# Performance work log

Hardware: AMD Instinct MI355X
Metric: run time of the kernel (lower is better)

Reference implementation:

```python
import jax, jax.numpy as jnp
import numpy as np

ROUTING_ITERS = 3

def _squash(s, axis=-1):
    # v = s * ||s||^2 / (1 + ||s||^2) / ||s||
    n2 = jnp.sum(s * s, axis=axis, keepdims=True)
    return s * n2 / (1.0 + n2) / jnp.sqrt(n2 + 1e-8)

def setup_inputs() -> dict:
    key = jax.random.key(0)
    k1, k2, k3 = jax.random.split(key, 3)
    B, R, C, O, I = 256, 1152, 10, 16, 8
    x = jax.random.normal(k1, (B, R, I), dtype=jnp.float32)
    W = jax.random.normal(k2, (R, C, O, I), dtype=jnp.float32) * 0.05
    bias = jax.random.normal(k3, (C, O), dtype=jnp.float32) * 0.05
    return {"x": x, "W": W, "bias": bias}

def reference(x, W, bias):
    # x: [B,R,I], W: [R,C,O,I], bias: [C,O]
    B = x.shape[0]
    R, C, O, I = W.shape
    # u_hat[b,r,c,o] = W[r,c,o,:] . x[b,r,:]   (torch: matmul(W, x) over broadcast batch)
    u_hat = jnp.einsum('rcoi,bri->brco', W, x)  # [B,R,C,O]
    b_ij = jnp.zeros((R, C), dtype=x.dtype)
    v = None
    for it in range(ROUTING_ITERS):
        c_ij = jax.nn.softmax(b_ij, axis=1)  # softmax over capsules (dim=2 in torch layout)
        s = jnp.einsum('rc,brco->bco', c_ij, u_hat) + bias  # [B,C,O]
        v = _squash(s, axis=-1)  # squash over out_channels (dim=-2 of [B,1,C,O,1])
        if it < ROUTING_ITERS - 1:
            # agreement: u_hat^T v, then mean over batch (keepdim collapses to shared logits)
            agree = jnp.einsum('brco,bco->brc', u_hat, v).mean(axis=0)  # [R,C]
            b_ij = b_ij + agree
    # torch returns v_j.squeeze(1): [B, C, O, 1]
    return v[..., None]
```

## Files before the change

### kernel.cpp

```cpp
#include <hip/hip_runtime.h>

#define CB 256
#define CR 1152
#define CC 10
#define CO 16
#define CI 8
#define CK (CR*CI)
#define NCO (CC*CO)

typedef __bf16 bf16_t;
typedef __attribute__((ext_vector_type(8))) __bf16 bf16x8;
typedef __attribute__((ext_vector_type(4))) float f32x4;

__global__ __launch_bounds__(256) void k_cvt(const float* __restrict__ x,
                                             const float* __restrict__ W,
                                             bf16_t* __restrict__ xb,
                                             bf16_t* __restrict__ xTb,
                                             bf16_t* __restrict__ Wt) {
  const int t = threadIdx.x;
  if (blockIdx.x < 1152) {
    const int bt = blockIdx.x & 7, kt = blockIdx.x >> 3;
    const int b0 = bt * 32, k0 = kt * 64;
    __shared__ float ldsT[64][33];
    const int row = t >> 3, cv = t & 7;
    const float4* xp = (const float4*)(x + (size_t)(b0 + row) * CK + k0 + cv * 8);
    const float4 f0 = xp[0], f1 = xp[1];
    float vals[8] = {f0.x, f0.y, f0.z, f0.w, f1.x, f1.y, f1.z, f1.w};
    bf16x8 ov;
    #pragma unroll
    for (int j = 0; j < 8; ++j) {
      ov[j] = (bf16_t)vals[j];
      ldsT[cv * 8 + j][row] = vals[j];
    }
    *(bf16x8*)(xb + (size_t)(b0 + row) * CK + k0 + cv * 8) = ov;
    __syncthreads();
    const int kr = t >> 2, bs = t & 3;
    bf16x8 tv;
    #pragma unroll
    for (int j = 0; j < 8; ++j) tv[j] = (bf16_t)ldsT[kr][bs * 8 + j];
    *(bf16x8*)(xTb + (size_t)(k0 + kr) * CB + b0 + bs * 8) = tv;
  } else {
    const int wi = (blockIdx.x - 1152) * 256 + t;
    const int r = wi % CR;
    const int co = wi / CR;
    const int c = co >> 4, o = co & 15;
    const float4* src = (const float4*)(W + (((size_t)r * CC + c) * CO + o) * CI);
    const float4 f0 = src[0], f1 = src[1];
    bf16x8 v;
    v[0] = (bf16_t)f0.x; v[1] = (bf16_t)f0.y; v[2] = (bf16_t)f0.z; v[3] = (bf16_t)f0.w;
    v[4] = (bf16_t)f1.x; v[5] = (bf16_t)f1.y; v[6] = (bf16_t)f1.z; v[7] = (bf16_t)f1.w;
    *(bf16x8*)(Wt + (size_t)co * CK + r * 8) = v;
  }
}

template<int MODE, bool LAST>
__global__ __launch_bounds__(1024) void k_s(const bf16_t* __restrict__ xb,
                                            const bf16_t* __restrict__ Bmat,
                                            const float* __restrict__ bias,
                                            bf16_t* __restrict__ vTb,
                                            float* __restrict__ out) {
  const int blk = blockIdx.x;
  const int xcd = blk & 7, j = blk >> 3;
  const int bt = xcd * 2 + (j & 1);
  const int c = j >> 1;
  const int t = threadIdx.x;
  const int w = t >> 6, lane = t & 63;
  const int mrow = lane & 15, kg = lane >> 4;
  const int b0 = bt * 16;
  const size_t kbase = (size_t)w * (CK / 16);

  const bf16x8* ap = (const bf16x8*)(xb + (size_t)(b0 + mrow) * CK + kbase) + kg;
  const bf16x8* bp = (const bf16x8*)(Bmat + (size_t)(c * CO + mrow) * CK + kbase) + kg;

  f32x4 acc0 = {0.f, 0.f, 0.f, 0.f}, acc1 = {0.f, 0.f, 0.f, 0.f};
  #pragma unroll
  for (int s = 0; s < 18; s += 2) {
    acc0 = __builtin_amdgcn_mfma_f32_16x16x32_bf16(ap[s * 4], bp[s * 4], acc0, 0, 0, 0);
    acc1 = __builtin_amdgcn_mfma_f32_16x16x32_bf16(ap[(s + 1) * 4], bp[(s + 1) * 4], acc1, 0, 0, 0);
  }
  const f32x4 acc = acc0 + acc1;

  __shared__ float Ls[16][64][4];
  #pragma unroll
  for (int reg = 0; reg < 4; ++reg) Ls[w][lane][reg] = acc[reg];
  __syncthreads();

  if (t < 256) {
    const int row = t >> 4, col = t & 15;
    const int l = ((row >> 2) << 4) | col, reg = row & 3;
    float s = 0.f;
    #pragma unroll
    for (int q = 0; q < 16; ++q) s += Ls[q][l][reg];
    if (MODE == 0) s *= 0.1f;
    s += bias[c * CO + col];
    float n2 = s * s;
    #pragma unroll
    for (int m = 1; m < 16; m <<= 1) n2 += __shfl_xor(n2, m);
    const float vv = s * n2 / (1.f + n2) * rsqrtf(n2 + 1e-8f);
    if (LAST) out[(size_t)(b0 + row) * NCO + c * CO + col] = vv;
    else      vTb[(size_t)(c * CO + col) * CB + b0 + row] = (bf16_t)vv;
  }
}

template<bool FIRST>
__global__ __launch_bounds__(512) void k_asc(const bf16_t* __restrict__ xTb,
                                             const bf16_t* __restrict__ vTb,
                                             const float* __restrict__ W,
                                             const bf16_t* __restrict__ Wt,
                                             float* __restrict__ b_ij,
                                             bf16_t* __restrict__ Wts) {
  const int r0 = blockIdx.x * 8;
  const int t = threadIdx.x;
  const int h = t >> 8;
  const int th = t & 255;
  const int w = th >> 6, lane = th & 63;
  const int mrow = lane & 15, kg = lane >> 4;

  __shared__ __align__(16) unsigned short vL[NCO][CB + 8];
  __shared__ float agrL[8][CC];
  __shared__ float cwL[8][CC];

  #pragma unroll
  for (int q = 0; q < 10; ++q) {
    const int idx = q * 512 + t;
    const int co = idx >> 5, bs = idx & 31;
    const bf16x8 v = ((const bf16x8*)vTb)[idx];
    *(bf16x8*)&vL[co][bs * 8] = v;
  }

  const int m0 = r0 * 8 + w * 16;
  const bf16x8* ap = (const bf16x8*)(xTb + (size_t)(m0 + mrow) * CB) + kg;
  bf16x8 a[8];
  #pragma unroll
  for (int s = 0; s < 8; ++s) a[s] = ap[s * 4];
  __syncthreads();

  const int o = lane & 15, g = lane >> 4;
  #pragma unroll
  for (int cc = 0; cc < 5; ++cc) {
    const int c = h * 5 + cc;
    f32x4 acc = {0.f, 0.f, 0.f, 0.f};
    #pragma unroll
    for (int s = 0; s < 8; ++s) {
      const bf16x8 bv = *(const bf16x8*)&vL[c * CO + mrow][s * 32 + kg * 8];
      acc = __builtin_amdgcn_mfma_f32_16x16x32_bf16(a[s], bv, acc, 0, 0, 0);
    }
    float p = 0.f;
    #pragma unroll
    for (int reg = 0; reg < 4; ++reg) {
      const int m = g * 4 + reg, rl = m >> 3, i = m & 7;
      p += acc[reg] * W[(((size_t)(r0 + w * 2 + rl) * CC + c) * CO + o) * CI + i];
    }
    #pragma unroll
    for (int msk = 1; msk < 32; msk <<= 1) p += __shfl_xor(p, msk);
    if ((lane & 31) == 0) agrL[w * 2 + (lane >> 5)][c] = p * (1.0f / CB);
  }
  __syncthreads();

  if (t < 8) {
    const int r = r0 + t;
    float nb[CC];
    float mx = -1e30f;
    #pragma unroll
    for (int c = 0; c < CC; ++c) {
      nb[c] = (FIRST ? 0.f : b_ij[r * CC + c]) + agrL[t][c];
      mx = fmaxf(mx, nb[c]);
    }
    float sum = 0.f;
    #pragma unroll
    for (int c = 0; c < CC; ++c) {
      b_ij[r * CC + c] = nb[c];
      const float e = __expf(nb[c] - mx);
      cwL[t][c] = e;
      sum += e;
    }
    const float inv = 1.f / sum;
    #pragma unroll
    for (int c = 0; c < CC; ++c) cwL[t][c] *= inv;
  }
  __syncthreads();

  #pragma unroll
  for (int q = 0; q < 3; ++q) {
    const int slot = q * 512 + t;
    if (slot < 1280) {
      const int co = slot >> 3, rl = slot & 7;
      const float cw = cwL[rl][co >> 4];
      const size_t off = (size_t)co * CK + (r0 + rl) * 8;
      const bf16x8 wv = *(const bf16x8*)(Wt + off);
      bf16x8 ov;
      #pragma unroll
      for (int jj = 0; jj < 8; ++jj) ov[jj] = (bf16_t)((float)wv[jj] * cw);
      *(bf16x8*)(Wts + off) = ov;
    }
  }
}

extern "C" void kernel_launch(void* const* d_in, const int* in_sizes, int n_in,
                              void* d_out, int out_size, void* d_ws, size_t ws_size,
                              hipStream_t stream) {
  const float* x    = (const float*)d_in[0];
  const float* W    = (const float*)d_in[1];
  const float* bias = (const float*)d_in[2];
  float* out = (float*)d_out;

  bf16_t* xb  = (bf16_t*)d_ws;
  bf16_t* xTb = xb  + (size_t)CB * CK;
  bf16_t* Wt  = xTb + (size_t)CB * CK;
  bf16_t* Wts = Wt  + (size_t)NCO * CK;
  bf16_t* vTb = Wts + (size_t)NCO * CK;
  float*  b_ij = (float*)(vTb + (size_t)NCO * CB);

  k_cvt<<<1872, 256, 0, stream>>>(x, W, xb, xTb, Wt);

  k_s<0, false><<<160, 1024, 0, stream>>>(xb, Wt, bias, vTb, out);
  k_asc<true><<<144, 512, 0, stream>>>(xTb, vTb, W, Wt, b_ij, Wts);

  k_s<1, false><<<160, 1024, 0, stream>>>(xb, Wts, bias, vTb, out);
  k_asc<false><<<144, 512, 0, stream>>>(xTb, vTb, W, Wt, b_ij, Wts);

  k_s<1, true><<<160, 1024, 0, stream>>>(xb, Wts, bias, vTb, out);
}
```

Baseline: 86.13 us.

## Fuse bf16 conversion into routing kernels and drop precomputed weight copies

New measurement: 103.9 us. +20.6%, slower.

```diff
diff --git a/kernel.cpp b/kernel.cpp
--- a/kernel.cpp
+++ b/kernel.cpp
@@ -12,75 +12,59 @@
 typedef __attribute__((ext_vector_type(8))) __bf16 bf16x8;
 typedef __attribute__((ext_vector_type(4))) float f32x4;
 
-__global__ __launch_bounds__(256) void k_cvt(const float* __restrict__ x,
-                                             const float* __restrict__ W,
-                                             bf16_t* __restrict__ xb,
-                                             bf16_t* __restrict__ xTb,
-                                             bf16_t* __restrict__ Wt) {
-  const int t = threadIdx.x;
-  if (blockIdx.x < 1152) {
-    const int bt = blockIdx.x & 7, kt = blockIdx.x >> 3;
-    const int b0 = bt * 32, k0 = kt * 64;
-    __shared__ float ldsT[64][33];
-    const int row = t >> 3, cv = t & 7;
-    const float4* xp = (const float4*)(x + (size_t)(b0 + row) * CK + k0 + cv * 8);
-    const float4 f0 = xp[0], f1 = xp[1];
-    float vals[8] = {f0.x, f0.y, f0.z, f0.w, f1.x, f1.y, f1.z, f1.w};
-    bf16x8 ov;
-    #pragma unroll
-    for (int j = 0; j < 8; ++j) {
-      ov[j] = (bf16_t)vals[j];
-      ldsT[cv * 8 + j][row] = vals[j];
-    }
-    *(bf16x8*)(xb + (size_t)(b0 + row) * CK + k0 + cv * 8) = ov;
-    __syncthreads();
-    const int kr = t >> 2, bs = t & 3;
-    bf16x8 tv;
-    #pragma unroll
-    for (int j = 0; j < 8; ++j) tv[j] = (bf16_t)ldsT[kr][bs * 8 + j];
-    *(bf16x8*)(xTb + (size_t)(k0 + kr) * CB + b0 + bs * 8) = tv;
-  } else {
-    const int wi = (blockIdx.x - 1152) * 256 + t;
-    const int r = wi % CR;
-    const int co = wi / CR;
-    const int c = co >> 4, o = co & 15;
-    const float4* src = (const float4*)(W + (((size_t)r * CC + c) * CO + o) * CI);
-    const float4 f0 = src[0], f1 = src[1];
-    bf16x8 v;
-    v[0] = (bf16_t)f0.x; v[1] = (bf16_t)f0.y; v[2] = (bf16_t)f0.z; v[3] = (bf16_t)f0.w;
-    v[4] = (bf16_t)f1.x; v[5] = (bf16_t)f1.y; v[6] = (bf16_t)f1.z; v[7] = (bf16_t)f1.w;
-    *(bf16x8*)(Wt + (size_t)co * CK + r * 8) = v;
-  }
+__device__ __forceinline__ unsigned short bfbits(float f) {
+  union { __bf16 h; unsigned short u; } u; u.h = (bf16_t)f; return u.u;
 }
 
 template<int MODE, bool LAST>
-__global__ __launch_bounds__(1024) void k_s(const bf16_t* __restrict__ xb,
-                                            const bf16_t* __restrict__ Bmat,
-                                            const float* __restrict__ bias,
-                                            bf16_t* __restrict__ vTb,
-                                            float* __restrict__ out) {
+__global__ __launch_bounds__(512) void k_s(const float* __restrict__ x,
+                                           const float* __restrict__ W,
+                                           const float* __restrict__ bias,
+                                           const float* __restrict__ cwT,
+                                           bf16_t* __restrict__ vTb,
+                                           float* __restrict__ out) {
   const int blk = blockIdx.x;
   const int xcd = blk & 7, j = blk >> 3;
-  const int bt = xcd * 2 + (j & 1);
-  const int c = j >> 1;
+  const int bt = (xcd & 3) * 4 + (j & 3);
+  const int c  = (xcd >> 2) * 5 + (j >> 2);
   const int t = threadIdx.x;
   const int w = t >> 6, lane = t & 63;
   const int mrow = lane & 15, kg = lane >> 4;
   const int b0 = bt * 16;
-  const size_t kbase = (size_t)w * (CK / 16);
 
-  const bf16x8* ap = (const bf16x8*)(xb + (size_t)(b0 + mrow) * CK + kbase) + kg;
-  const bf16x8* bp = (const bf16x8*)(Bmat + (size_t)(c * CO + mrow) * CK + kbase) + kg;
+  __shared__ float cwS[CR];
+  __shared__ float Ls[8][64][4];
+  if (MODE == 1) {
+    if (t < CR / 4) ((float4*)cwS)[t] = ((const float4*)(cwT + (size_t)c * CR))[t];
+    __syncthreads();
+  }
 
-  f32x4 acc0 = {0.f, 0.f, 0.f, 0.f}, acc1 = {0.f, 0.f, 0.f, 0.f};
-  #pragma unroll
-  for (int s = 0; s < 18; s += 2) {
-    acc0 = __builtin_amdgcn_mfma_f32_16x16x32_bf16(ap[s * 4], bp[s * 4], acc0, 0, 0, 0);
-    acc1 = __builtin_amdgcn_mfma_f32_16x16x32_bf16(ap[(s + 1) * 4], bp[(s + 1) * 4], acc1, 0, 0, 0);
+  const int r0w = w * 144;
+  const float4* ax = (const float4*)(x + (size_t)(b0 + mrow) * CK + (size_t)w * 1152) + kg * 2;
+
+  f32x4 acc = {0.f, 0.f, 0.f, 0.f};
+  #pragma unroll 4
+  for (int s = 0; s < 36; ++s) {
+    const float4 a0 = ax[s * 8], a1 = ax[s * 8 + 1];
+    const int r = r0w + s * 4 + kg;
+    const float4* wp = (const float4*)(W + (((size_t)r * CC + c) * CO + mrow) * CI);
+    const float4 w0 = wp[0], w1 = wp[1];
+    bf16x8 af, bf;
+    af[0] = (bf16_t)a0.x; af[1] = (bf16_t)a0.y; af[2] = (bf16_t)a0.z; af[3] = (bf16_t)a0.w;
+    af[4] = (bf16_t)a1.x; af[5] = (bf16_t)a1.y; af[6] = (bf16_t)a1.z; af[7] = (bf16_t)a1.w;
+    if (MODE == 1) {
+      const float cw = cwS[r];
+      bf[0] = (bf16_t)(w0.x * cw); bf[1] = (bf16_t)(w0.y * cw);
+      bf[2] = (bf16_t)(w0.z * cw); bf[3] = (bf16_t)(w0.w * cw);
+      bf[4] = (bf16_t)(w1.x * cw); bf[5] = (bf16_t)(w1.y * cw);
+      bf[6] = (bf16_t)(w1.z * cw); bf[7] = (bf16_t)(w1.w * cw);
+    } else {
+      bf[0] = (bf16_t)w0.x; bf[1] = (bf16_t)w0.y; bf[2] = (bf16_t)w0.z; bf[3] = (bf16_t)w0.w;
+      bf[4] = (bf16_t)w1.x; bf[5] = (bf16_t)w1.y; bf[6] = (bf16_t)w1.z; bf[7] = (bf16_t)w1.w;
+    }
+    acc = __builtin_amdgcn_mfma_f32_16x16x32_bf16(af, bf, acc, 0, 0, 0);
   }
-  const f32x4 acc = acc0 + acc1;
 
-  __shared__ float Ls[16][64][4];
   #pragma unroll
   for (int reg = 0; reg < 4; ++reg) Ls[w][lane][reg] = acc[reg];
   __syncthreads();
@@ -90,7 +74,7 @@
     const int l = ((row >> 2) << 4) | col, reg = row & 3;
     float s = 0.f;
     #pragma unroll
-    for (int q = 0; q < 16; ++q) s += Ls[q][l][reg];
+    for (int q = 0; q < 8; ++q) s += Ls[q][l][reg];
     if (MODE == 0) s *= 0.1f;
     s += bias[c * CO + col];
     float n2 = s * s;
@@ -103,12 +87,11 @@
 }
 
 template<bool FIRST>
-__global__ __launch_bounds__(512) void k_asc(const bf16_t* __restrict__ xTb,
+__global__ __launch_bounds__(512) void k_asc(const float* __restrict__ x,
+                                             const float* __restrict__ W,
                                              const bf16_t* __restrict__ vTb,
-                                             const float* __restrict__ W,
-                                             const bf16_t* __restrict__ Wt,
                                              float* __restrict__ b_ij,
-                                             bf16_t* __restrict__ Wts) {
+                                             float* __restrict__ cwT) {
   const int r0 = blockIdx.x * 8;
   const int t = threadIdx.x;
   const int h = t >> 8;
@@ -117,6 +100,7 @@
   const int mrow = lane & 15, kg = lane >> 4;
 
   __shared__ __align__(16) unsigned short vL[NCO][CB + 8];
+  __shared__ __align__(16) unsigned short xTl[64][CB + 8];
   __shared__ float agrL[8][CC];
   __shared__ float cwL[8][CC];
 
@@ -127,13 +111,20 @@
     const bf16x8 v = ((const bf16x8*)vTb)[idx];
     *(bf16x8*)&vL[co][bs * 8] = v;
   }
+  #pragma unroll
+  for (int chunk = 0; chunk < 16; ++chunk) {
+    const int b = chunk * 16 + (t >> 5);
+    const int ri = (t & 31) * 2;
+    const float2 v = *(const float2*)(x + (size_t)b * CK + r0 * 8 + ri);
+    xTl[ri][b] = bfbits(v.x);
+    xTl[ri + 1][b] = bfbits(v.y);
+  }
+  __syncthreads();
 
-  const int m0 = r0 * 8 + w * 16;
-  const bf16x8* ap = (const bf16x8*)(xTb + (size_t)(m0 + mrow) * CB) + kg;
   bf16x8 a[8];
   #pragma unroll
-  for (int s = 0; s < 8; ++s) a[s] = ap[s * 4];
-  __syncthreads();
+  for (int s = 0; s < 8; ++s)
+    a[s] = *(const bf16x8*)&xTl[w * 16 + mrow][s * 32 + kg * 8];
 
   const int o = lane & 15, g = lane >> 4;
   #pragma unroll
@@ -176,23 +167,7 @@
     }
     const float inv = 1.f / sum;
     #pragma unroll
-    for (int c = 0; c < CC; ++c) cwL[t][c] *= inv;
-  }
-  __syncthreads();
-
-  #pragma unroll
-  for (int q = 0; q < 3; ++q) {
-    const int slot = q * 512 + t;
-    if (slot < 1280) {
-      const int co = slot >> 3, rl = slot & 7;
-      const float cw = cwL[rl][co >> 4];
-      const size_t off = (size_t)co * CK + (r0 + rl) * 8;
-      const bf16x8 wv = *(const bf16x8*)(Wt + off);
-      bf16x8 ov;
-      #pragma unroll
-      for (int jj = 0; jj < 8; ++jj) ov[jj] = (bf16_t)((float)wv[jj] * cw);
-      *(bf16x8*)(Wts + off) = ov;
-    }
+    for (int c = 0; c < CC; ++c) cwT[(size_t)c * CR + r] = cwL[t][c] * inv;
   }
 }
 
@@ -204,20 +179,15 @@
   const float* bias = (const float*)d_in[2];
   float* out = (float*)d_out;
 
-  bf16_t* xb  = (bf16_t*)d_ws;
-  bf16_t* xTb = xb  + (size_t)CB * CK;
-  bf16_t* Wt  = xTb + (size_t)CB * CK;
-  bf16_t* Wts = Wt  + (size_t)NCO * CK;
-  bf16_t* vTb = Wts + (size_t)NCO * CK;
+  bf16_t* vTb  = (bf16_t*)d_ws;
   float*  b_ij = (float*)(vTb + (size_t)NCO * CB);
+  float*  cwT  = b_ij + (size_t)CR * CC;
 
-  k_cvt<<<1872, 256, 0, stream>>>(x, W, xb, xTb, Wt);
+  k_s<0, false><<<160, 512, 0, stream>>>(x, W, bias, cwT, vTb, out);
+  k_asc<true><<<144, 512, 0, stream>>>(x, W, vTb, b_ij, cwT);
 
-  k_s<0, false><<<160, 1024, 0, stream>>>(xb, Wt, bias, vTb, out);
-  k_asc<true><<<144, 512, 0, stream>>>(xTb, vTb, W, Wt, b_ij, Wts);
+  k_s<1, false><<<160, 512, 0, stream>>>(x, W, bias, cwT, vTb, out);
+  k_asc<false><<<144, 512, 0, stream>>>(x, W, vTb, b_ij, cwT);
 
-  k_s<1, false><<<160, 1024, 0, stream>>>(xb, Wts, bias, vTb, out);
-  k_asc<false><<<144, 512, 0, stream>>>(xTb, vTb, W, Wt, b_ij, Wts);
-
-  k_s<1, true><<<160, 1024, 0, stream>>>(xb, Wts, bias, vTb, out);
+  k_s<1, true><<<160, 512, 0, stream>>>(x, W, bias, cwT, vTb, out);
 }
```

## Drop global transposed x copy; transpose x into LDS inside agreement kernel

Applied to the files above, without the earlier changes.

Measured after the change: 85.14 us. No clear change (-1.1%).

```diff
diff --git a/kernel.cpp b/kernel.cpp
--- a/kernel.cpp
+++ b/kernel.cpp
@@ -12,39 +12,28 @@
 typedef __attribute__((ext_vector_type(8))) __bf16 bf16x8;
 typedef __attribute__((ext_vector_type(4))) float f32x4;
 
+__device__ __forceinline__ unsigned short bfbits(float f) {
+  union { __bf16 h; unsigned short u; } u; u.h = (bf16_t)f; return u.u;
+}
+
 __global__ __launch_bounds__(256) void k_cvt(const float* __restrict__ x,
                                              const float* __restrict__ W,
                                              bf16_t* __restrict__ xb,
-                                             bf16_t* __restrict__ xTb,
                                              bf16_t* __restrict__ Wt) {
-  const int t = threadIdx.x;
-  if (blockIdx.x < 1152) {
-    const int bt = blockIdx.x & 7, kt = blockIdx.x >> 3;
-    const int b0 = bt * 32, k0 = kt * 64;
-    __shared__ float ldsT[64][33];
-    const int row = t >> 3, cv = t & 7;
-    const float4* xp = (const float4*)(x + (size_t)(b0 + row) * CK + k0 + cv * 8);
-    const float4 f0 = xp[0], f1 = xp[1];
-    float vals[8] = {f0.x, f0.y, f0.z, f0.w, f1.x, f1.y, f1.z, f1.w};
-    bf16x8 ov;
-    #pragma unroll
-    for (int j = 0; j < 8; ++j) {
-      ov[j] = (bf16_t)vals[j];
-      ldsT[cv * 8 + j][row] = vals[j];
-    }
-    *(bf16x8*)(xb + (size_t)(b0 + row) * CK + k0 + cv * 8) = ov;
-    __syncthreads();
-    const int kr = t >> 2, bs = t & 3;
-    bf16x8 tv;
-    #pragma unroll
-    for (int j = 0; j < 8; ++j) tv[j] = (bf16_t)ldsT[kr][bs * 8 + j];
-    *(bf16x8*)(xTb + (size_t)(k0 + kr) * CB + b0 + bs * 8) = tv;
+  const int idx = blockIdx.x * 256 + threadIdx.x;
+  const int NX = CB * CK / 8;
+  if (idx < NX) {
+    const float4 f0 = ((const float4*)x)[idx * 2];
+    const float4 f1 = ((const float4*)x)[idx * 2 + 1];
+    bf16x8 o;
+    o[0] = (bf16_t)f0.x; o[1] = (bf16_t)f0.y; o[2] = (bf16_t)f0.z; o[3] = (bf16_t)f0.w;
+    o[4] = (bf16_t)f1.x; o[5] = (bf16_t)f1.y; o[6] = (bf16_t)f1.z; o[7] = (bf16_t)f1.w;
+    ((bf16x8*)xb)[idx] = o;
   } else {
-    const int wi = (blockIdx.x - 1152) * 256 + t;
-    const int r = wi % CR;
-    const int co = wi / CR;
-    const int c = co >> 4, o = co & 15;
-    const float4* src = (const float4*)(W + (((size_t)r * CC + c) * CO + o) * CI);
+    const int wi = idx - NX;
+    const int co = wi % NCO;
+    const int r  = wi / NCO;
+    const float4* src = (const float4*)(W + ((size_t)r * NCO + co) * CI);
     const float4 f0 = src[0], f1 = src[1];
     bf16x8 v;
     v[0] = (bf16_t)f0.x; v[1] = (bf16_t)f0.y; v[2] = (bf16_t)f0.z; v[3] = (bf16_t)f0.w;
@@ -67,11 +56,9 @@
   const int w = t >> 6, lane = t & 63;
   const int mrow = lane & 15, kg = lane >> 4;
   const int b0 = bt * 16;
-  const size_t kbase = (size_t)w * (CK / 16);
-
-  const bf16x8* ap = (const bf16x8*)(xb + (size_t)(b0 + mrow) * CK + kbase) + kg;
-  const bf16x8* bp = (const bf16x8*)(Bmat + (size_t)(c * CO + mrow) * CK + kbase) + kg;
-
+
+  const bf16x8* ap = (const bf16x8*)(xb + (size_t)(b0 + mrow) * CK + w * 576) + kg;
+  const bf16x8* bp = (const bf16x8*)(Bmat + ((size_t)c * CO + mrow) * CK + w * 576) + kg;
   f32x4 acc0 = {0.f, 0.f, 0.f, 0.f}, acc1 = {0.f, 0.f, 0.f, 0.f};
   #pragma unroll
   for (int s = 0; s < 18; s += 2) {
@@ -84,7 +71,6 @@
   #pragma unroll
   for (int reg = 0; reg < 4; ++reg) Ls[w][lane][reg] = acc[reg];
   __syncthreads();
-
   if (t < 256) {
     const int row = t >> 4, col = t & 15;
     const int l = ((row >> 2) << 4) | col, reg = row & 3;
@@ -103,9 +89,9 @@
 }
 
 template<bool FIRST>
-__global__ __launch_bounds__(512) void k_asc(const bf16_t* __restrict__ xTb,
+__global__ __launch_bounds__(512) void k_asc(const float* __restrict__ x,
+                                             const float* __restrict__ W,
                                              const bf16_t* __restrict__ vTb,
-                                             const float* __restrict__ W,
                                              const bf16_t* __restrict__ Wt,
                                              float* __restrict__ b_ij,
                                              bf16_t* __restrict__ Wts) {
@@ -117,6 +103,7 @@
   const int mrow = lane & 15, kg = lane >> 4;
 
   __shared__ __align__(16) unsigned short vL[NCO][CB + 8];
+  __shared__ __align__(16) unsigned short xTl[64][CB + 8];
   __shared__ float agrL[8][CC];
   __shared__ float cwL[8][CC];
 
@@ -127,13 +114,20 @@
     const bf16x8 v = ((const bf16x8*)vTb)[idx];
     *(bf16x8*)&vL[co][bs * 8] = v;
   }
-
-  const int m0 = r0 * 8 + w * 16;
-  const bf16x8* ap = (const bf16x8*)(xTb + (size_t)(m0 + mrow) * CB) + kg;
+  #pragma unroll
+  for (int chunk = 0; chunk < 16; ++chunk) {
+    const int b = chunk * 16 + (t >> 5);
+    const int ri = (t & 31) * 2;
+    const float2 v = *(const float2*)(x + (size_t)b * CK + r0 * 8 + ri);
+    xTl[ri][b] = bfbits(v.x);
+    xTl[ri + 1][b] = bfbits(v.y);
+  }
+  __syncthreads();
+
   bf16x8 a[8];
   #pragma unroll
-  for (int s = 0; s < 8; ++s) a[s] = ap[s * 4];
-  __syncthreads();
+  for (int s = 0; s < 8; ++s)
+    a[s] = *(const bf16x8*)&xTl[w * 16 + mrow][s * 32 + kg * 8];
 
   const int o = lane & 15, g = lane >> 4;
   #pragma unroll
@@ -205,19 +199,18 @@
   float* out = (float*)d_out;
 
   bf16_t* xb  = (bf16_t*)d_ws;
-  bf16_t* xTb = xb  + (size_t)CB * CK;
-  bf16_t* Wt  = xTb + (size_t)CB * CK;
+  bf16_t* Wt  = xb  + (size_t)CB * CK;
   bf16_t* Wts = Wt  + (size_t)NCO * CK;
   bf16_t* vTb = Wts + (size_t)NCO * CK;
   float*  b_ij = (float*)(vTb + (size_t)NCO * CB);
 
-  k_cvt<<<1872, 256, 0, stream>>>(x, W, xb, xTb, Wt);
+  k_cvt<<<1872, 256, 0, stream>>>(x, W, xb, Wt);
 
   k_s<0, false><<<160, 1024, 0, stream>>>(xb, Wt, bias, vTb, out);
-  k_asc<true><<<144, 512, 0, stream>>>(xTb, vTb, W, Wt, b_ij, Wts);
+  k_asc<true><<<144, 512, 0, stream>>>(x, W, vTb, Wt, b_ij, Wts);
 
   k_s<1, false><<<160, 1024, 0, stream>>>(xb, Wts, bias, vTb, out);
-  k_asc<false><<<144, 512, 0, stream>>>(xTb, vTb, W, Wt, b_ij, Wts);
+  k_asc<false><<<144, 512, 0, stream>>>(x, W, vTb, Wt, b_ij, Wts);
 
   k_s<1, true><<<160, 1024, 0, stream>>>(xb, Wts, bias, vTb, out);
 }
```
